# Kernel optimization log

Hardware: AMD Instinct MI355X
Metric: run time of the kernel (lower is better)

The kernel has to match this reference:

```python
import jax, jax.numpy as jnp
import numpy as np

D_MODEL = 64
D_STATE = 16
HEADDIM = 16
D_INNER = 128            # expand * d_model
N_HEADS = D_INNER // HEADDIM  # 8
N_LAYERS = 2
EMB = 8
CONV_K = 4
N_ACTIONS = 6
N_AGG = 10
XBC = D_INNER + 2 * D_STATE   # 160
IN_W = 2 * D_INNER + 2 * D_STATE + N_HEADS  # 296


def setup_inputs() -> dict:
    key = jax.random.key(0)
    ks = jax.random.split(key, 16)
    B, L = 16, 2048
    s = 0.02
    inp = {
        "aggs": jax.random.randint(ks[0], (B, L, N_AGG), 0, 3),
        "peg_E": jax.random.normal(ks[1], (3, EMB), jnp.float32) * s,
        "count_E": jax.random.normal(ks[2], (18, EMB), jnp.float32) * s,
        "top_E": jax.random.normal(ks[3], (17, EMB), jnp.float32) * s,
        "proj_in_w": jax.random.normal(ks[4], (N_AGG * EMB, D_MODEL), jnp.float32) * s,
        "proj_in_b": jnp.zeros((D_MODEL,), jnp.float32),
        "rms_w": jnp.ones((N_LAYERS, D_MODEL), jnp.float32),
        "in_w": jax.random.normal(ks[5], (N_LAYERS, D_MODEL, IN_W), jnp.float32) * s,
        "conv_w": jax.random.normal(ks[6], (N_LAYERS, XBC, CONV_K), jnp.float32) * s,
        "conv_b": jnp.zeros((N_LAYERS, XBC), jnp.float32),
        "dt_bias": jax.random.normal(ks[7], (N_LAYERS, N_HEADS), jnp.float32) * s,
        "A_log": jnp.log(jax.random.uniform(ks[8], (N_LAYERS, N_HEADS), jnp.float32, 1.0, 4.0)),
        "Dp": jnp.ones((N_LAYERS, N_HEADS), jnp.float32),
        "outp_w": jax.random.normal(ks[9], (N_LAYERS, D_INNER, D_MODEL), jnp.float32) * s,
        "ln_g": jnp.ones((D_MODEL,), jnp.float32),
        "ln_b": jnp.zeros((D_MODEL,), jnp.float32),
        "out_w": jax.random.normal(ks[10], (D_MODEL, N_ACTIONS), jnp.float32) * s,
        "out_b": jnp.zeros((N_ACTIONS,), jnp.float32),
    }
    return inp


def _silu(x):
    return x * jax.nn.sigmoid(x)


def _rope(v, cos, sin):
    # v: [B,L,N]; rotate-half RoPE over the d_state dim
    h = v.shape[-1] // 2
    v1, v2 = v[..., :h], v[..., h:]
    return jnp.concatenate([v1 * cos - v2 * sin, v1 * sin + v2 * cos], axis=-1)


def _block(x, rms_w, in_w, conv_w, conv_b, dt_bias, A_log, Dp, outp_w):
    B, L, _ = x.shape
    # RMSNorm
    xn = x * jax.lax.rsqrt(jnp.mean(x * x, axis=-1, keepdims=True) + 1e-6) * rms_w
    zxbcdt = xn @ in_w  # [B,L,296]
    z = zxbcdt[..., :D_INNER]
    xbc = zxbcdt[..., D_INNER:D_INNER + XBC]
    dt_raw = zxbcdt[..., D_INNER + XBC:]  # [B,L,H]
    # causal depthwise conv (kernel 4) + silu on (x,B,C)
    w = jnp.transpose(conv_w)[:, None, :]  # [K,1,XBC]
    xbc = jax.lax.conv_general_dilated(
        xbc, w, (1,), [(CONV_K - 1, 0)], feature_group_count=XBC,
        dimension_numbers=("NWC", "WIO", "NWC")) + conv_b
    xbc = _silu(xbc)
    xs = xbc[..., :D_INNER].reshape(B, L, N_HEADS, HEADDIM)
    Bm = xbc[..., D_INNER:D_INNER + D_STATE]
    Cm = xbc[..., D_INNER + D_STATE:]
    # RoPE on B and C
    half = D_STATE // 2
    inv_freq = 1.0 / (10000.0 ** (jnp.arange(half, dtype=jnp.float32) / half))
    ang = jnp.arange(L, dtype=jnp.float32)[:, None] * inv_freq  # [L,half]
    cos, sin = jnp.cos(ang), jnp.sin(ang)
    Bm, Cm = _rope(Bm, cos, sin), _rope(Cm, cos, sin)
    # discretization
    dt = jax.nn.softplus(dt_raw + dt_bias)          # [B,L,H]
    a = jnp.exp(dt * (-jnp.exp(A_log)))             # [B,L,H], decay in (0,1)
    # trapezoidal selective scan over time
    def step(carry, inp):
        h, Bx_prev = carry
        x_t, B_t, C_t, dt_t, a_t = inp
        Bx = jnp.einsum("bhp,bn->bhpn", x_t, B_t)
        ae = a_t[..., None, None]
        h = ae * h + 0.5 * dt_t[..., None, None] * (Bx + ae * Bx_prev)
        y = jnp.einsum("bhpn,bn->bhp", h, C_t)
        return (h, Bx), y

    h0 = jnp.zeros((B, N_HEADS, HEADDIM, D_STATE), x.dtype)
    init = (h0, h0)
    seq = (xs.transpose(1, 0, 2, 3), Bm.transpose(1, 0, 2), Cm.transpose(1, 0, 2),
           dt.transpose(1, 0, 2), a.transpose(1, 0, 2))
    _, ys = jax.lax.scan(step, init, seq)
    y = ys.transpose(1, 0, 2, 3) + Dp[None, None, :, None] * xs  # [B,L,H,P]
    y = y.reshape(B, L, D_INNER) * _silu(z)
    return y @ outp_w


def reference(aggs, peg_E, count_E, top_E, proj_in_w, proj_in_b, rms_w, in_w,
              conv_w, conv_b, dt_bias, A_log, Dp, outp_w, ln_g, ln_b, out_w, out_b):
    tables = [peg_E, peg_E, count_E, count_E, count_E, top_E, top_E, top_E, count_E, peg_E]
    e = jnp.concatenate([tables[i][aggs[..., i]] for i in range(N_AGG)], axis=-1)
    x = e @ proj_in_w + proj_in_b
    for l in range(N_LAYERS):
        x = x + _block(x, rms_w[l], in_w[l], conv_w[l], conv_b[l],
                       dt_bias[l], A_log[l], Dp[l], outp_w[l])
    mu = jnp.mean(x, axis=-1, keepdims=True)
    var = jnp.mean((x - mu) ** 2, axis=-1, keepdims=True)
    x = (x - mu) * jax.lax.rsqrt(var + 1e-5) * ln_g + ln_b
    return x @ out_w + out_b
```

## Files before the change

kernel.cpp:

```cpp
#include <hip/hip_runtime.h>
#include <hip/hip_bf16.h>

#define B_    16
#define L_    2048
#define BL    (B_ * L_)
#define DM    64
#define DS    16
#define HD    16
#define DI    128
#define NH    8
#define INW   296
#define XBC_  160
#define CONVK 4
#define NAGG  10
#define NACT  6
#define CS    128
#define NC    (L_ / CS)

__global__ __launch_bounds__(256) void k_embed(
    const int* __restrict__ aggs, const float* __restrict__ pegE,
    const float* __restrict__ countE, const float* __restrict__ topE,
    const float* __restrict__ W, const float* __restrict__ bias,
    float* __restrict__ x) {
  __shared__ float e[16][80];
  const int row0 = blockIdx.x * 16;
  const int t = threadIdx.x;
  if (t < 160) {
    int r = t / 10, i = t % 10;
    const float* tab = (i == 0 || i == 1 || i == 9) ? pegE
                       : (i >= 5 && i <= 7)         ? topE
                                                    : countE;
    int idx = aggs[(row0 + r) * NAGG + i];
    const float* src = tab + idx * 8;
#pragma unroll
    for (int j = 0; j < 8; ++j) e[r][i * 8 + j] = src[j];
  }
  __syncthreads();
  const int c = t & 63, rg = t >> 6;
  float acc[4] = {0.f, 0.f, 0.f, 0.f};
  for (int k = 0; k < 80; ++k) {
    float wk = W[k * 64 + c];
#pragma unroll
    for (int j = 0; j < 4; ++j) acc[j] += e[rg + j * 4][k] * wk;
  }
  float bc = bias[c];
#pragma unroll
  for (int j = 0; j < 4; ++j) x[(row0 + rg + j * 4) * 64 + c] = acc[j] + bc;
}

__global__ __launch_bounds__(256) void k_inproj(
    const float* __restrict__ x, const float* __restrict__ rms_w,
    const float* __restrict__ W, float* __restrict__ out) {
  __shared__ float xn[16][64];
  const int row0 = blockIdx.x * 16;
  const int t = threadIdx.x;
  const int r = t >> 4, l = t & 15;
  float v[4];
  float ss = 0.f;
#pragma unroll
  for (int j = 0; j < 4; ++j) {
    v[j] = x[(row0 + r) * 64 + l * 4 + j];
    ss += v[j] * v[j];
  }
#pragma unroll
  for (int o = 1; o < 16; o <<= 1) ss += __shfl_xor(ss, o, 64);
  float inv = rsqrtf(ss * (1.0f / 64.0f) + 1e-6f);
#pragma unroll
  for (int j = 0; j < 4; ++j) xn[r][l * 4 + j] = v[j] * inv * rms_w[l * 4 + j];
  __syncthreads();
  for (int c = t; c < INW; c += 256) {
    float acc[16];
#pragma unroll
    for (int r2 = 0; r2 < 16; ++r2) acc[r2] = 0.f;
    for (int k = 0; k < 64; ++k) {
      float wk = W[k * INW + c];
#pragma unroll
      for (int r2 = 0; r2 < 16; ++r2) acc[r2] += xn[r2][k] * wk;
    }
#pragma unroll
    for (int r2 = 0; r2 < 16; ++r2) out[(row0 + r2) * INW + c] = acc[r2];
  }
}

__global__ __launch_bounds__(256) void k_conv(
    const float* __restrict__ zx, const float* __restrict__ conv_w,
    const float* __restrict__ conv_b, const float* __restrict__ dt_bias,
    const float* __restrict__ A_log, float* __restrict__ xs,
    float* __restrict__ Bmr, float* __restrict__ Cmr,
    float* __restrict__ a_arr, float* __restrict__ hd_arr) {
  __shared__ float bc[16][32];
  const int row0 = blockIdx.x * 16;
  const int t = threadIdx.x;
  for (int idx = t; idx < 16 * XBC_; idx += 256) {
    int c = idx % XBC_;
    int rr = idx / XBC_;
    int row = row0 + rr;
    int tpos = row & (L_ - 1);
    float acc = conv_b[c];
#pragma unroll
    for (int k = 0; k < CONVK; ++k) {
      int tt = tpos - 3 + k;
      if (tt >= 0) acc += zx[(row - 3 + k) * INW + 128 + c] * conv_w[c * 4 + k];
    }
    float s = acc / (1.0f + __expf(-acc));
    if (c < 128)
      xs[row * 128 + c] = s;
    else
      bc[rr][c - 128] = s;
  }
  __syncthreads();
  {
    int rr = t >> 4, j = t & 15;
    int row = row0 + rr;
    int tpos = row & (L_ - 1);
    int i = j & 7;
    float invf = powf(10000.0f, -(float)i * 0.125f);
    float ang = (float)tpos * invf;
    float sn = sinf(ang), cs = cosf(ang);
    if (j < 8) {
      float b1 = bc[rr][i], b2 = bc[rr][i + 8];
      Bmr[row * 16 + i] = b1 * cs - b2 * sn;
      Bmr[row * 16 + i + 8] = b1 * sn + b2 * cs;
    } else {
      float c1 = bc[rr][16 + i], c2 = bc[rr][24 + i];
      Cmr[row * 16 + i] = c1 * cs - c2 * sn;
      Cmr[row * 16 + i + 8] = c1 * sn + c2 * cs;
    }
  }
  if (t < 128) {
    int rr = t >> 3, h = t & 7;
    int row = row0 + rr;
    float dtr = zx[row * INW + 288 + h] + dt_bias[h];
    float dt = log1pf(expf(dtr));
    float a = expf(-expf(A_log[h]) * dt);
    a_arr[row * 8 + h] = a;
    hd_arr[row * 8 + h] = 0.5f * dt;
  }
}

__global__ __launch_bounds__(64) void k_scan1(
    const float* __restrict__ xs, const float* __restrict__ Bmr,
    const float* __restrict__ Cmr, const float* __restrict__ a_arr,
    const float* __restrict__ hd_arr, float* __restrict__ yloc,
    float* __restrict__ cum_arr, float* __restrict__ hend,
    float* __restrict__ aprod) {
  const int bid = blockIdx.x;
  const int ck = bid % NC, bh = bid / NC;
  const int h = bh % NH, b = bh / NH;
  const int lane = threadIdx.x;
  const int p = lane >> 2, ng = lane & 3;
  const int rowbase = b * L_;
  const int t0 = ck * CS;

  float hst[4] = {0.f, 0.f, 0.f, 0.f};
  float bxp[4] = {0.f, 0.f, 0.f, 0.f};
  if (t0 > 0) {
    int rp = rowbase + t0 - 1;
    float xp = xs[rp * 128 + h * 16 + p];
    float4 Bp = *(const float4*)(Bmr + rp * 16 + ng * 4);
    bxp[0] = xp * Bp.x;
    bxp[1] = xp * Bp.y;
    bxp[2] = xp * Bp.z;
    bxp[3] = xp * Bp.w;
  }
  float cum = 1.0f;
  for (int i = 0; i < CS; ++i) {
    const int row = rowbase + t0 + i;
    float xv = xs[row * 128 + h * 16 + p];
    float4 Bv = *(const float4*)(Bmr + row * 16 + ng * 4);
    float4 Cv = *(const float4*)(Cmr + row * 16 + ng * 4);
    float av = a_arr[row * 8 + h];
    float hd = hd_arr[row * 8 + h];
    float bx[4] = {xv * Bv.x, xv * Bv.y, xv * Bv.z, xv * Bv.w};
    float y = 0.f;
    float C[4] = {Cv.x, Cv.y, Cv.z, Cv.w};
#pragma unroll
    for (int j = 0; j < 4; ++j) {
      hst[j] = av * hst[j] + hd * (bx[j] + av * bxp[j]);
      y += hst[j] * C[j];
      bxp[j] = bx[j];
    }
    cum *= av;
    y += __shfl_xor(y, 1, 64);
    y += __shfl_xor(y, 2, 64);
    if (ng == 0) yloc[row * 128 + h * 16 + p] = y;
    if (lane == 0) cum_arr[row * 8 + h] = cum;
  }
  const int cbase = (bh * NC + ck) * 256;
#pragma unroll
  for (int j = 0; j < 4; ++j) hend[cbase + p * 16 + ng * 4 + j] = hst[j];
  if (lane == 0) aprod[bh * NC + ck] = cum;
}

__global__ __launch_bounds__(256) void k_scan2(const float* __restrict__ hend,
                                               const float* __restrict__ aprod,
                                               float* __restrict__ hstart) {
  const int bh = blockIdx.x;
  const int t = threadIdx.x;
  float hs = 0.f;
  for (int c = 0; c < NC; ++c) {
    hstart[(bh * NC + c) * 256 + t] = hs;
    hs = aprod[bh * NC + c] * hs + hend[(bh * NC + c) * 256 + t];
  }
}

__global__ __launch_bounds__(256) void k_out(
    const float* __restrict__ yloc, const float* __restrict__ cum_arr,
    const float* __restrict__ hstart, const float* __restrict__ Cmr,
    const float* __restrict__ xs, const float* __restrict__ zx,
    const float* __restrict__ Dp, const float* __restrict__ W,
    float* __restrict__ x) {
  __shared__ float g[16][128];
  const int row0 = blockIdx.x * 16;
  const int t = threadIdx.x;
  const int b = row0 / L_;
  const int ck = (row0 & (L_ - 1)) / CS;
  for (int idx = t; idx < 16 * 128; idx += 256) {
    int hp = idx & 127, rr = idx >> 7;
    int row = row0 + rr;
    int hh = hp >> 4, p = hp & 15;
    const float* hs = hstart + ((b * NH + hh) * NC + ck) * 256 + p * 16;
    const float* C = Cmr + row * 16;
    float dot = 0.f;
#pragma unroll
    for (int n = 0; n < 16; ++n) dot += hs[n] * C[n];
    float y = yloc[row * 128 + hp] + cum_arr[row * 8 + hh] * dot +
              Dp[hh] * xs[row * 128 + hp];
    float zv = zx[row * INW + hp];
    g[rr][hp] = y * (zv / (1.0f + __expf(-zv)));
  }
  __syncthreads();
  const int c = t & 63, rg = t >> 6;
  float acc[4] = {0.f, 0.f, 0.f, 0.f};
  for (int k = 0; k < 128; ++k) {
    float wk = W[k * 64 + c];
#pragma unroll
    for (int j = 0; j < 4; ++j) acc[j] += g[rg + j * 4][k] * wk;
  }
#pragma unroll
  for (int j = 0; j < 4; ++j) {
    int row = row0 + rg + j * 4;
    x[row * 64 + c] += acc[j];
  }
}

__global__ __launch_bounds__(256) void k_head(
    const float* __restrict__ x, const float* __restrict__ ln_g,
    const float* __restrict__ ln_b, const float* __restrict__ W,
    const float* __restrict__ bias, float* __restrict__ out) {
  __shared__ float xn[4][64];
  const int t = threadIdx.x;
  const int r = t >> 6, k = t & 63;
  const int row = blockIdx.x * 4 + r;
  float v = x[row * 64 + k];
  float mu = v;
#pragma unroll
  for (int o = 1; o < 64; o <<= 1) mu += __shfl_xor(mu, o, 64);
  mu *= (1.0f / 64.0f);
  float d = v - mu;
  float var = d * d;
#pragma unroll
  for (int o = 1; o < 64; o <<= 1) var += __shfl_xor(var, o, 64);
  var *= (1.0f / 64.0f);
  xn[r][k] = d * rsqrtf(var + 1e-5f) * ln_g[k] + ln_b[k];
  __syncthreads();
  if (k < NACT) {
    float acc = bias[k];
    for (int kk = 0; kk < 64; ++kk) acc += xn[r][kk] * W[kk * NACT + k];
    out[row * NACT + k] = acc;
  }
}

extern "C" void kernel_launch(void* const* d_in, const int* in_sizes, int n_in,
                              void* d_out, int out_size, void* d_ws,
                              size_t ws_size, hipStream_t stream) {
  const int* aggs = (const int*)d_in[0];
  const float* pegE = (const float*)d_in[1];
  const float* countE = (const float*)d_in[2];
  const float* topE = (const float*)d_in[3];
  const float* proj_in_w = (const float*)d_in[4];
  const float* proj_in_b = (const float*)d_in[5];
  const float* rms_w = (const float*)d_in[6];
  const float* in_w = (const float*)d_in[7];
  const float* conv_w = (const float*)d_in[8];
  const float* conv_b = (const float*)d_in[9];
  const float* dt_bias = (const float*)d_in[10];
  const float* A_log = (const float*)d_in[11];
  const float* Dp = (const float*)d_in[12];
  const float* outp_w = (const float*)d_in[13];
  const float* ln_g = (const float*)d_in[14];
  const float* ln_b = (const float*)d_in[15];
  const float* out_w = (const float*)d_in[16];
  const float* out_b = (const float*)d_in[17];
  float* out = (float*)d_out;

  float* ws = (float*)d_ws;
  size_t off = 0;
  float* x = ws + off;       off += (size_t)BL * 64;
  float* zx = ws + off;      off += (size_t)BL * INW;
  float* xs = ws + off;      off += (size_t)BL * 128;
  float* Bmr = ws + off;     off += (size_t)BL * 16;
  float* Cmr = ws + off;     off += (size_t)BL * 16;
  float* a_arr = ws + off;   off += (size_t)BL * 8;
  float* hd_arr = ws + off;  off += (size_t)BL * 8;
  float* yloc = ws + off;    off += (size_t)BL * 128;
  float* cum_arr = ws + off; off += (size_t)BL * 8;
  float* hend = ws + off;    off += (size_t)B_ * NH * NC * 256;
  float* aprod = ws + off;   off += (size_t)B_ * NH * NC;
  float* hstart = ws + off;  off += (size_t)B_ * NH * NC * 256;

  k_embed<<<BL / 16, 256, 0, stream>>>(aggs, pegE, countE, topE, proj_in_w,
                                       proj_in_b, x);
  for (int l = 0; l < 2; ++l) {
    k_inproj<<<BL / 16, 256, 0, stream>>>(x, rms_w + l * 64,
                                          in_w + (size_t)l * 64 * INW, zx);
    k_conv<<<BL / 16, 256, 0, stream>>>(zx, conv_w + l * XBC_ * 4,
                                        conv_b + l * XBC_, dt_bias + l * 8,
                                        A_log + l * 8, xs, Bmr, Cmr, a_arr,
                                        hd_arr);
    k_scan1<<<B_ * NH * NC, 64, 0, stream>>>(xs, Bmr, Cmr, a_arr, hd_arr, yloc,
                                             cum_arr, hend, aprod);
    k_scan2<<<B_ * NH, 256, 0, stream>>>(hend, aprod, hstart);
    k_out<<<BL / 16, 256, 0, stream>>>(yloc, cum_arr, hstart, Cmr, xs, zx,
                                       Dp + l * 8, outp_w + (size_t)l * 128 * 64,
                                       x);
  }
  k_head<<<BL / 4, 256, 0, stream>>>(x, ln_g, ln_b, out_w, out_b, out);
}
```

Baseline: 428.1 us.

## Halve scan chunk, pack scan tasks per block, prefetch loads, vectorize GEMM loops

The scan chunk size drops from 128 to 64, and four chunk tasks are packed into each 256-thread block so the sequential scan has twice the parallelism. The scan loop software-prefetches the next step's inputs, and the a and dt arrays are merged into one float2 array. The conv kernel stages its input rows and weights in shared memory. The small GEMM loops are unrolled by four with float4 shared-memory reads and explicit FMAs, and several expf/powf calls become fast intrinsics. The smaller chunk doubles the hend/hstart traffic and the serial length of scan2. The fast intrinsics and the softplus cutoff slightly change numerics.

```diff
diff --git a/kernel.cpp b/kernel.cpp
--- a/kernel.cpp
+++ b/kernel.cpp
@@ -14,7 +14,7 @@
 #define CONVK 4
 #define NAGG  10
 #define NACT  6
-#define CS    128
+#define CS    64
 #define NC    (L_ / CS)
 
 __global__ __launch_bounds__(256) void k_embed(
@@ -38,14 +38,22 @@
   __syncthreads();
   const int c = t & 63, rg = t >> 6;
   float acc[4] = {0.f, 0.f, 0.f, 0.f};
-  for (int k = 0; k < 80; ++k) {
-    float wk = W[k * 64 + c];
-#pragma unroll
-    for (int j = 0; j < 4; ++j) acc[j] += e[rg + j * 4][k] * wk;
+  const float* Wc = W + c;
+  for (int k = 0; k < 80; k += 4) {
+    float w0 = Wc[k * 64], w1 = Wc[(k + 1) * 64], w2 = Wc[(k + 2) * 64],
+          w3 = Wc[(k + 3) * 64];
+#pragma unroll
+    for (int j = 0; j < 4; ++j) {
+      float4 ev = *(const float4*)&e[rg + j * 4][k];
+      acc[j] = fmaf(ev.x, w0, acc[j]);
+      acc[j] = fmaf(ev.y, w1, acc[j]);
+      acc[j] = fmaf(ev.z, w2, acc[j]);
+      acc[j] = fmaf(ev.w, w3, acc[j]);
+    }
   }
   float bc = bias[c];
 #pragma unroll
-  for (int j = 0; j < 4; ++j) x[(row0 + rg + j * 4) * 64 + c] = acc[j] + bc;
+  for (int j = 0; j < 4; ++j) x[(size_t)(row0 + rg + j * 4) * 64 + c] = acc[j] + bc;
 }
 
 __global__ __launch_bounds__(256) void k_inproj(
@@ -55,30 +63,35 @@
   const int row0 = blockIdx.x * 16;
   const int t = threadIdx.x;
   const int r = t >> 4, l = t & 15;
-  float v[4];
-  float ss = 0.f;
-#pragma unroll
-  for (int j = 0; j < 4; ++j) {
-    v[j] = x[(row0 + r) * 64 + l * 4 + j];
-    ss += v[j] * v[j];
-  }
+  float4 v = *(const float4*)&x[(size_t)(row0 + r) * 64 + l * 4];
+  float ss = v.x * v.x + v.y * v.y + v.z * v.z + v.w * v.w;
 #pragma unroll
   for (int o = 1; o < 16; o <<= 1) ss += __shfl_xor(ss, o, 64);
   float inv = rsqrtf(ss * (1.0f / 64.0f) + 1e-6f);
-#pragma unroll
-  for (int j = 0; j < 4; ++j) xn[r][l * 4 + j] = v[j] * inv * rms_w[l * 4 + j];
+  xn[r][l * 4 + 0] = v.x * inv * rms_w[l * 4 + 0];
+  xn[r][l * 4 + 1] = v.y * inv * rms_w[l * 4 + 1];
+  xn[r][l * 4 + 2] = v.z * inv * rms_w[l * 4 + 2];
+  xn[r][l * 4 + 3] = v.w * inv * rms_w[l * 4 + 3];
   __syncthreads();
   for (int c = t; c < INW; c += 256) {
     float acc[16];
 #pragma unroll
     for (int r2 = 0; r2 < 16; ++r2) acc[r2] = 0.f;
-    for (int k = 0; k < 64; ++k) {
-      float wk = W[k * INW + c];
-#pragma unroll
-      for (int r2 = 0; r2 < 16; ++r2) acc[r2] += xn[r2][k] * wk;
-    }
-#pragma unroll
-    for (int r2 = 0; r2 < 16; ++r2) out[(row0 + r2) * INW + c] = acc[r2];
+    const float* Wc = W + c;
+    for (int k = 0; k < 64; k += 4) {
+      float w0 = Wc[k * INW], w1 = Wc[(k + 1) * INW], w2 = Wc[(k + 2) * INW],
+            w3 = Wc[(k + 3) * INW];
+#pragma unroll
+      for (int r2 = 0; r2 < 16; ++r2) {
+        float4 xv = *(const float4*)&xn[r2][k];
+        acc[r2] = fmaf(xv.x, w0, acc[r2]);
+        acc[r2] = fmaf(xv.y, w1, acc[r2]);
+        acc[r2] = fmaf(xv.z, w2, acc[r2]);
+        acc[r2] = fmaf(xv.w, w3, acc[r2]);
+      }
+    }
+#pragma unroll
+    for (int r2 = 0; r2 < 16; ++r2) out[(size_t)(row0 + r2) * INW + c] = acc[r2];
   }
 }
 
@@ -87,24 +100,33 @@
     const float* __restrict__ conv_b, const float* __restrict__ dt_bias,
     const float* __restrict__ A_log, float* __restrict__ xs,
     float* __restrict__ Bmr, float* __restrict__ Cmr,
-    float* __restrict__ a_arr, float* __restrict__ hd_arr) {
+    float2* __restrict__ ahd) {
+  __shared__ float s_zx[19][160];
+  __shared__ float s_cw[640];
+  __shared__ float s_cb[160];
   __shared__ float bc[16][32];
   const int row0 = blockIdx.x * 16;
   const int t = threadIdx.x;
+  for (int idx = t; idx < 19 * 160; idx += 256) {
+    int rr = idx / 160, c = idx - rr * 160;
+    int row = row0 - 3 + rr;
+    s_zx[rr][c] = (row >= 0) ? zx[(size_t)row * INW + 128 + c] : 0.f;
+  }
+  for (int idx = t; idx < 640; idx += 256) s_cw[idx] = conv_w[idx];
+  if (t < 160) s_cb[t] = conv_b[t];
+  __syncthreads();
   for (int idx = t; idx < 16 * XBC_; idx += 256) {
-    int c = idx % XBC_;
-    int rr = idx / XBC_;
+    int rr = idx / 160, c = idx - rr * 160;
     int row = row0 + rr;
     int tpos = row & (L_ - 1);
-    float acc = conv_b[c];
+    float acc = s_cb[c];
 #pragma unroll
     for (int k = 0; k < CONVK; ++k) {
-      int tt = tpos - 3 + k;
-      if (tt >= 0) acc += zx[(row - 3 + k) * INW + 128 + c] * conv_w[c * 4 + k];
+      if (tpos - 3 + k >= 0) acc = fmaf(s_zx[rr + k][c], s_cw[c * 4 + k], acc);
     }
     float s = acc / (1.0f + __expf(-acc));
     if (c < 128)
-      xs[row * 128 + c] = s;
+      xs[(size_t)row * 128 + c] = s;
     else
       bc[rr][c - 128] = s;
   }
@@ -114,82 +136,114 @@
     int row = row0 + rr;
     int tpos = row & (L_ - 1);
     int i = j & 7;
-    float invf = powf(10000.0f, -(float)i * 0.125f);
+    float invf = exp2f(-(float)i * 1.66096404744368f);
     float ang = (float)tpos * invf;
     float sn = sinf(ang), cs = cosf(ang);
     if (j < 8) {
       float b1 = bc[rr][i], b2 = bc[rr][i + 8];
-      Bmr[row * 16 + i] = b1 * cs - b2 * sn;
-      Bmr[row * 16 + i + 8] = b1 * sn + b2 * cs;
+      Bmr[(size_t)row * 16 + i] = b1 * cs - b2 * sn;
+      Bmr[(size_t)row * 16 + i + 8] = b1 * sn + b2 * cs;
     } else {
       float c1 = bc[rr][16 + i], c2 = bc[rr][24 + i];
-      Cmr[row * 16 + i] = c1 * cs - c2 * sn;
-      Cmr[row * 16 + i + 8] = c1 * sn + c2 * cs;
+      Cmr[(size_t)row * 16 + i] = c1 * cs - c2 * sn;
+      Cmr[(size_t)row * 16 + i + 8] = c1 * sn + c2 * cs;
     }
   }
   if (t < 128) {
     int rr = t >> 3, h = t & 7;
     int row = row0 + rr;
-    float dtr = zx[row * INW + 288 + h] + dt_bias[h];
-    float dt = log1pf(expf(dtr));
-    float a = expf(-expf(A_log[h]) * dt);
-    a_arr[row * 8 + h] = a;
-    hd_arr[row * 8 + h] = 0.5f * dt;
-  }
-}
-
-__global__ __launch_bounds__(64) void k_scan1(
+    float dtr = zx[(size_t)row * INW + 288 + h] + dt_bias[h];
+    float dt = (dtr > 20.f) ? dtr : log1pf(__expf(dtr));
+    float a = __expf(-__expf(A_log[h]) * dt);
+    ahd[(size_t)row * 8 + h] = make_float2(a, 0.5f * dt);
+  }
+}
+
+__device__ __forceinline__ void scan_step(float xv, const float Bb[4],
+                                          const float Cb[4], float2 ah,
+                                          float hst[4], float bxp[4],
+                                          float& cum, float& yout) {
+  float av = ah.x, hd = ah.y;
+  float y = 0.f;
+#pragma unroll
+  for (int j = 0; j < 4; ++j) {
+    float bx = xv * Bb[j];
+    float t1 = fmaf(hd, bxp[j], hst[j]);
+    hst[j] = fmaf(av, t1, hd * bx);
+    y = fmaf(hst[j], Cb[j], y);
+    bxp[j] = bx;
+  }
+  cum *= av;
+  yout = y;
+}
+
+__global__ __launch_bounds__(256) void k_scan1(
     const float* __restrict__ xs, const float* __restrict__ Bmr,
-    const float* __restrict__ Cmr, const float* __restrict__ a_arr,
-    const float* __restrict__ hd_arr, float* __restrict__ yloc,
-    float* __restrict__ cum_arr, float* __restrict__ hend,
-    float* __restrict__ aprod) {
-  const int bid = blockIdx.x;
-  const int ck = bid % NC, bh = bid / NC;
-  const int h = bh % NH, b = bh / NH;
-  const int lane = threadIdx.x;
+    const float* __restrict__ Cmr, const float2* __restrict__ ahd,
+    float* __restrict__ yloc, float* __restrict__ cum_arr,
+    float* __restrict__ hend, float* __restrict__ aprod) {
+  const int task = blockIdx.x * 4 + (threadIdx.x >> 6);
+  const int ck = task & (NC - 1), bh = task >> 5;
+  const int h = bh & 7, b = bh >> 3;
+  const int lane = threadIdx.x & 63;
   const int p = lane >> 2, ng = lane & 3;
-  const int rowbase = b * L_;
   const int t0 = ck * CS;
+  const int row0 = b * L_ + t0;
+
+  const float* xp = xs + (size_t)row0 * 128 + h * 16 + p;
+  const float* Bp = Bmr + (size_t)row0 * 16 + ng * 4;
+  const float* Cp = Cmr + (size_t)row0 * 16 + ng * 4;
+  const float2* ap = ahd + (size_t)row0 * 8 + h;
+  float* ylp = yloc + (size_t)row0 * 128 + h * 16 + p;
+  float* cp = cum_arr + (size_t)row0 * 8 + h;
 
   float hst[4] = {0.f, 0.f, 0.f, 0.f};
   float bxp[4] = {0.f, 0.f, 0.f, 0.f};
   if (t0 > 0) {
-    int rp = rowbase + t0 - 1;
-    float xp = xs[rp * 128 + h * 16 + p];
-    float4 Bp = *(const float4*)(Bmr + rp * 16 + ng * 4);
-    bxp[0] = xp * Bp.x;
-    bxp[1] = xp * Bp.y;
-    bxp[2] = xp * Bp.z;
-    bxp[3] = xp * Bp.w;
+    float xprev = xp[-128];
+    float Bprev[4];
+    *(float4*)Bprev = *(const float4*)(Bp - 16);
+#pragma unroll
+    for (int j = 0; j < 4; ++j) bxp[j] = xprev * Bprev[j];
   }
   float cum = 1.0f;
-  for (int i = 0; i < CS; ++i) {
-    const int row = rowbase + t0 + i;
-    float xv = xs[row * 128 + h * 16 + p];
-    float4 Bv = *(const float4*)(Bmr + row * 16 + ng * 4);
-    float4 Cv = *(const float4*)(Cmr + row * 16 + ng * 4);
-    float av = a_arr[row * 8 + h];
-    float hd = hd_arr[row * 8 + h];
-    float bx[4] = {xv * Bv.x, xv * Bv.y, xv * Bv.z, xv * Bv.w};
-    float y = 0.f;
-    float C[4] = {Cv.x, Cv.y, Cv.z, Cv.w};
-#pragma unroll
-    for (int j = 0; j < 4; ++j) {
-      hst[j] = av * hst[j] + hd * (bx[j] + av * bxp[j]);
-      y += hst[j] * C[j];
-      bxp[j] = bx[j];
-    }
-    cum *= av;
+  float xv = xp[0];
+  float Bb[4], Cb[4];
+  *(float4*)Bb = *(const float4*)Bp;
+  *(float4*)Cb = *(const float4*)Cp;
+  float2 ah = ap[0];
+
+  for (int i = 0; i < CS - 1; ++i) {
+    float xv2 = xp[(size_t)(i + 1) * 128];
+    float Bb2[4], Cb2[4];
+    *(float4*)Bb2 = *(const float4*)(Bp + (i + 1) * 16);
+    *(float4*)Cb2 = *(const float4*)(Cp + (i + 1) * 16);
+    float2 ah2 = ap[(size_t)(i + 1) * 8];
+    float y;
+    scan_step(xv, Bb, Cb, ah, hst, bxp, cum, y);
     y += __shfl_xor(y, 1, 64);
     y += __shfl_xor(y, 2, 64);
-    if (ng == 0) yloc[row * 128 + h * 16 + p] = y;
-    if (lane == 0) cum_arr[row * 8 + h] = cum;
-  }
-  const int cbase = (bh * NC + ck) * 256;
-#pragma unroll
-  for (int j = 0; j < 4; ++j) hend[cbase + p * 16 + ng * 4 + j] = hst[j];
-  if (lane == 0) aprod[bh * NC + ck] = cum;
+    if (ng == 0) ylp[(size_t)i * 128] = y;
+    if (lane == 0) cp[(size_t)i * 8] = cum;
+    xv = xv2;
+    ah = ah2;
+#pragma unroll
+    for (int j = 0; j < 4; ++j) {
+      Bb[j] = Bb2[j];
+      Cb[j] = Cb2[j];
+    }
+  }
+  {
+    float y;
+    scan_step(xv, Bb, Cb, ah, hst, bxp, cum, y);
+    y += __shfl_xor(y, 1, 64);
+    y += __shfl_xor(y, 2, 64);
+    if (ng == 0) ylp[(size_t)(CS - 1) * 128] = y;
+    if (lane == 0) cp[(size_t)(CS - 1) * 8] = cum;
+  }
+  float4 hv = make_float4(hst[0], hst[1], hst[2], hst[3]);
+  *(float4*)(hend + (size_t)task * 256 + p * 16 + ng * 4) = hv;
+  if (lane == 0) aprod[task] = cum;
 }
 
 __global__ __launch_bounds__(256) void k_scan2(const float* __restrict__ hend,
@@ -197,10 +251,20 @@
                                                float* __restrict__ hstart) {
   const int bh = blockIdx.x;
   const int t = threadIdx.x;
+  const float* he = hend + (size_t)bh * NC * 256 + t;
+  const float* apr = aprod + bh * NC;
+  float* hsp = hstart + (size_t)bh * NC * 256 + t;
   float hs = 0.f;
+  float hn = he[0];
+  float ap = apr[0];
   for (int c = 0; c < NC; ++c) {
-    hstart[(bh * NC + c) * 256 + t] = hs;
-    hs = aprod[bh * NC + c] * hs + hend[(bh * NC + c) * 256 + t];
+    int c1 = (c + 1 < NC) ? c + 1 : c;
+    float hn2 = he[(size_t)c1 * 256];
+    float ap2 = apr[c1];
+    hsp[(size_t)c * 256] = hs;
+    hs = fmaf(ap, hs, hn);
+    hn = hn2;
+    ap = ap2;
   }
 }
 
@@ -219,28 +283,40 @@
     int hp = idx & 127, rr = idx >> 7;
     int row = row0 + rr;
     int hh = hp >> 4, p = hp & 15;
-    const float* hs = hstart + ((b * NH + hh) * NC + ck) * 256 + p * 16;
-    const float* C = Cmr + row * 16;
-    float dot = 0.f;
-#pragma unroll
-    for (int n = 0; n < 16; ++n) dot += hs[n] * C[n];
-    float y = yloc[row * 128 + hp] + cum_arr[row * 8 + hh] * dot +
-              Dp[hh] * xs[row * 128 + hp];
-    float zv = zx[row * INW + hp];
+    const float4* hs =
+        (const float4*)(hstart + ((size_t)(b * NH + hh) * NC + ck) * 256 + p * 16);
+    const float4* C4 = (const float4*)(Cmr + (size_t)row * 16);
+    float4 h0 = hs[0], h1 = hs[1], h2 = hs[2], h3 = hs[3];
+    float4 c0 = C4[0], c1 = C4[1], c2 = C4[2], c3 = C4[3];
+    float dot = h0.x * c0.x + h0.y * c0.y + h0.z * c0.z + h0.w * c0.w +
+                h1.x * c1.x + h1.y * c1.y + h1.z * c1.z + h1.w * c1.w +
+                h2.x * c2.x + h2.y * c2.y + h2.z * c2.z + h2.w * c2.w +
+                h3.x * c3.x + h3.y * c3.y + h3.z * c3.z + h3.w * c3.w;
+    float y = yloc[(size_t)row * 128 + hp] + cum_arr[(size_t)row * 8 + hh] * dot +
+              Dp[hh] * xs[(size_t)row * 128 + hp];
+    float zv = zx[(size_t)row * INW + hp];
     g[rr][hp] = y * (zv / (1.0f + __expf(-zv)));
   }
   __syncthreads();
   const int c = t & 63, rg = t >> 6;
   float acc[4] = {0.f, 0.f, 0.f, 0.f};
-  for (int k = 0; k < 128; ++k) {
-    float wk = W[k * 64 + c];
-#pragma unroll
-    for (int j = 0; j < 4; ++j) acc[j] += g[rg + j * 4][k] * wk;
+  const float* Wc = W + c;
+  for (int k = 0; k < 128; k += 4) {
+    float w0 = Wc[k * 64], w1 = Wc[(k + 1) * 64], w2 = Wc[(k + 2) * 64],
+          w3 = Wc[(k + 3) * 64];
+#pragma unroll
+    for (int j = 0; j < 4; ++j) {
+      float4 gv = *(const float4*)&g[rg + j * 4][k];
+      acc[j] = fmaf(gv.x, w0, acc[j]);
+      acc[j] = fmaf(gv.y, w1, acc[j]);
+      acc[j] = fmaf(gv.z, w2, acc[j]);
+      acc[j] = fmaf(gv.w, w3, acc[j]);
+    }
   }
 #pragma unroll
   for (int j = 0; j < 4; ++j) {
     int row = row0 + rg + j * 4;
-    x[row * 64 + c] += acc[j];
+    x[(size_t)row * 64 + c] += acc[j];
   }
 }
 
@@ -252,7 +328,7 @@
   const int t = threadIdx.x;
   const int r = t >> 6, k = t & 63;
   const int row = blockIdx.x * 4 + r;
-  float v = x[row * 64 + k];
+  float v = x[(size_t)row * 64 + k];
   float mu = v;
 #pragma unroll
   for (int o = 1; o < 64; o <<= 1) mu += __shfl_xor(mu, o, 64);
@@ -266,8 +342,8 @@
   __syncthreads();
   if (k < NACT) {
     float acc = bias[k];
-    for (int kk = 0; kk < 64; ++kk) acc += xn[r][kk] * W[kk * NACT + k];
-    out[row * NACT + k] = acc;
+    for (int kk = 0; kk < 64; ++kk) acc = fmaf(xn[r][kk], W[kk * NACT + k], acc);
+    out[(size_t)row * NACT + k] = acc;
   }
 }
 
@@ -301,8 +377,7 @@
   float* xs = ws + off;      off += (size_t)BL * 128;
   float* Bmr = ws + off;     off += (size_t)BL * 16;
   float* Cmr = ws + off;     off += (size_t)BL * 16;
-  float* a_arr = ws + off;   off += (size_t)BL * 8;
-  float* hd_arr = ws + off;  off += (size_t)BL * 8;
+  float2* ahd = (float2*)(ws + off); off += (size_t)BL * 16;
   float* yloc = ws + off;    off += (size_t)BL * 128;
   float* cum_arr = ws + off; off += (size_t)BL * 8;
   float* hend = ws + off;    off += (size_t)B_ * NH * NC * 256;
@@ -316,10 +391,9 @@
                                           in_w + (size_t)l * 64 * INW, zx);
     k_conv<<<BL / 16, 256, 0, stream>>>(zx, conv_w + l * XBC_ * 4,
                                         conv_b + l * XBC_, dt_bias + l * 8,
-                                        A_log + l * 8, xs, Bmr, Cmr, a_arr,
-                                        hd_arr);
-    k_scan1<<<B_ * NH * NC, 64, 0, stream>>>(xs, Bmr, Cmr, a_arr, hd_arr, yloc,
-                                             cum_arr, hend, aprod);
+                                        A_log + l * 8, xs, Bmr, Cmr, ahd);
+    k_scan1<<<B_ * NH * NC / 4, 256, 0, stream>>>(xs, Bmr, Cmr, ahd, yloc,
+                                                  cum_arr, hend, aprod);
     k_scan2<<<B_ * NH, 256, 0, stream>>>(hend, aprod, hstart);
     k_out<<<BL / 16, 256, 0, stream>>>(yloc, cum_arr, hstart, Cmr, xs, zx,
                                        Dp + l * 8, outp_w + (size_t)l * 128 * 64,
```

Result: faster. 371.1 us (-13.3%).
